# Performance work log

Measured on AMD Instinct MI355X. Metric: run time of the kernel, lower is better.

Reference implementation:

```python
import jax, jax.numpy as jnp
import numpy as np

B, S, D = 4, 2048, 1024
E, K, H = 8, 2, 2048  # experts, top_k, swiglu hidden (ff_multiplier=2.0)
EPS = 1e-8
RMS_EPS = 1e-6
ROPE_BASE = 10000.0


def setup_inputs() -> dict:
    key = jax.random.key(0)
    ks = jax.random.split(key, 6)
    scale_in = 1.0 / np.sqrt(D)
    scale_h = 1.0 / np.sqrt(H)
    return {
        "x": jax.random.normal(ks[0], (B, S, D), jnp.float32),
        "norm_w": jnp.ones((D,), jnp.float32),
        "router_W": jax.random.normal(ks[1], (E, D), jnp.float32) * scale_in,  # nn.Linear weight [E,D]
        "w1": jax.random.normal(ks[2], (E, H, D), jnp.float32) * scale_in,  # gate proj per expert
        "w3": jax.random.normal(ks[3], (E, H, D), jnp.float32) * scale_in,  # up proj per expert
        "w2": jax.random.normal(ks[4], (E, D, H), jnp.float32) * scale_h,   # down proj per expert
    }


def _rmsnorm(x, w):
    var = jnp.mean(jnp.square(x), axis=-1, keepdims=True)
    return x * jax.lax.rsqrt(var + RMS_EPS) * w


def _rope(x):
    # half-split rotary embedding over full embed dim; x: [B,S,D]
    d2 = D // 2
    inv_freq = 1.0 / (ROPE_BASE ** (jnp.arange(0, d2, dtype=jnp.float32) / d2))
    ang = jnp.arange(S, dtype=jnp.float32)[:, None] * inv_freq[None, :]  # [S,D/2]
    cos, sin = jnp.cos(ang), jnp.sin(ang)
    x1, x2 = x[..., :d2], x[..., d2:]
    return jnp.concatenate([x1 * cos - x2 * sin, x1 * sin + x2 * cos], axis=-1)


def reference(x, norm_w, router_W, w1, w3, w2):
    hidden = _rope(_rmsnorm(x, norm_w))  # [B,S,D]
    logits = jnp.einsum("bsd,ed->bse", hidden, router_W)
    probs = jax.nn.softmax(logits, axis=-1)
    # sparse top-k renormalized gates
    top_v, top_i = jax.lax.top_k(probs, K)  # [B,S,K]
    sparse = jnp.sum(jax.nn.one_hot(top_i, E, dtype=probs.dtype) * top_v[..., None], axis=-2)  # [B,S,E]
    gates = sparse / jnp.clip(jnp.sum(sparse, axis=-1, keepdims=True), EPS)
    # dense all-expert SwiGLU
    g = jnp.einsum("bsd,ehd->bseh", hidden, w1)
    u = jnp.einsum("bsd,ehd->bseh", hidden, w3)
    act = jax.nn.silu(g) * u
    expert_out = jnp.einsum("bseh,edh->bsed", act, w2)  # [B,S,E,D]
    mixed = jnp.sum(gates[..., None] * expert_out, axis=-2)
    return mixed + x
```

## Files before the change

kernel.cpp:

```cpp
#include <hip/hip_runtime.h>

#define TOKENS 8192
#define Dm 1024
#define Hm 2048
#define Sm 2048
#define D2 512
#define SLOTS 16384
#define PADU 256
#define SLOTPAD (SLOTS + 8*PADU)
#define NWE 16777216

#define OF_TAB 0ull
#define OF_HID (OF_TAB + (size_t)Sm*D2*8)
#define OF_ACT (OF_HID + (size_t)TOKENS*Dm*2)
#define OF_W1B (OF_ACT + (size_t)SLOTPAD*Hm*2)
#define OF_W3B (OF_W1B + (size_t)NWE*2)
#define OF_W2B (OF_W3B + (size_t)NWE*2)
#define OF_T2I (OF_W2B + (size_t)NWE*2)
#define OF_T2G (OF_T2I + (size_t)TOKENS*2*4)
#define OF_T2S (OF_T2G + (size_t)TOKENS*2*4)
#define OF_ST  (OF_T2S + (size_t)TOKENS*2*4)
#define OF_SG  (OF_ST + (size_t)SLOTPAD*4)
#define OF_MT  (OF_SG + (size_t)SLOTPAD*4)
#define OF_SO  (OF_MT + 1024)

typedef __bf16 bf16x8 __attribute__((ext_vector_type(8)));
typedef short  s16x8  __attribute__((ext_vector_type(8)));
typedef float  f32x4  __attribute__((ext_vector_type(4)));

__device__ __forceinline__ unsigned short f2bf(float f) {
    union { float f; unsigned u; } v; v.f = f;
    unsigned r = v.u + 0x7fffu + ((v.u >> 16) & 1u);
    return (unsigned short)(r >> 16);
}

__device__ __forceinline__ float bf2f(unsigned short u) {
    union { unsigned u; float f; } v; v.u = ((unsigned)u) << 16;
    return v.f;
}

__device__ __forceinline__ f32x4 mfma16(s16x8 a, s16x8 b, f32x4 c) {
    return __builtin_amdgcn_mfma_f32_16x16x32_bf16(
        __builtin_bit_cast(bf16x8, a), __builtin_bit_cast(bf16x8, b), c, 0, 0, 0);
}

__device__ __forceinline__ void gld16(const void* g, void* l) {
    __builtin_amdgcn_global_load_lds(
        (const __attribute__((address_space(1))) void*)g,
        (__attribute__((address_space(3))) void*)l, 16, 0, 0);
}

__device__ __forceinline__ int xcd_swz(int bid, int nwg) {
    int cpx = nwg >> 3;
    return (bid & 7) * cpx + (bid >> 3);
}

__global__ void k_init(int* slot_token, int* meta) {
    int i = blockIdx.x * 256 + threadIdx.x;
    if (i < SLOTPAD) slot_token[i] = -1;
    if (i < 8) meta[i] = 0;
}

__global__ __launch_bounds__(256) void k_convert3(
    const float* __restrict__ w1, const float* __restrict__ w3,
    const float* __restrict__ w2, unsigned short* __restrict__ d1,
    unsigned short* __restrict__ d3, unsigned short* __restrict__ d2)
{
    size_t i = ((size_t)blockIdx.x * 256 + threadIdx.x) * 8;
    const float* s; unsigned short* d;
    if (i < (size_t)NWE)            { s = w1; d = d1; }
    else if (i < 2ull * NWE)        { s = w3; d = d3; i -= (size_t)NWE; }
    else                            { s = w2; d = d2; i -= 2ull * NWE; }
    float4 a = *(const float4*)(s + i);
    float4 b = *(const float4*)(s + i + 4);
    s16x8 v;
    v[0]=(short)f2bf(a.x); v[1]=(short)f2bf(a.y); v[2]=(short)f2bf(a.z); v[3]=(short)f2bf(a.w);
    v[4]=(short)f2bf(b.x); v[5]=(short)f2bf(b.y); v[6]=(short)f2bf(b.z); v[7]=(short)f2bf(b.w);
    *(s16x8*)(d + i) = v;
}

__global__ void k_table(float2* tab) {
    int i = blockIdx.x * 256 + threadIdx.x;
    int s = i >> 9, j = i & 511;
    float inv = expf(-(float)j * (9.210340371976184f / 512.0f));
    float ang = (float)s * inv;
    tab[i] = make_float2(cosf(ang), sinf(ang));
}

__global__ __launch_bounds__(256) void k_token(
    const float* __restrict__ x, const float* __restrict__ nw,
    const float* __restrict__ rW, const float2* __restrict__ tab,
    unsigned short* __restrict__ hid,
    int* __restrict__ t2i, float* __restrict__ t2g)
{
    int t = blockIdx.x;
    int tid = threadIdx.x;
    int lane = tid & 63, wid = tid >> 6;
    int s = t & (Sm - 1);
    const float* xr = x + (size_t)t * Dm;

    float v0 = xr[tid], v1 = xr[tid + 256], v2 = xr[tid + 512], v3 = xr[tid + 768];
    float ss = v0*v0 + v1*v1 + v2*v2 + v3*v3;
    #pragma unroll
    for (int o = 32; o; o >>= 1) ss += __shfl_down(ss, o);
    __shared__ float red[4];
    if (lane == 0) red[wid] = ss;
    __syncthreads();
    float tot = red[0] + red[1] + red[2] + red[3];
    float rms = rsqrtf(tot * (1.0f / Dm) + 1e-6f);

    float n0 = v0 * rms * nw[tid];
    float n1 = v1 * rms * nw[tid + 256];
    float n2 = v2 * rms * nw[tid + 512];
    float n3 = v3 * rms * nw[tid + 768];

    float2 c0 = tab[s * D2 + tid];
    float2 c1 = tab[s * D2 + tid + 256];
    float h0 = n0 * c0.x - n2 * c0.y;
    float h2 = n0 * c0.y + n2 * c0.x;
    float h1 = n1 * c1.x - n3 * c1.y;
    float h3 = n1 * c1.y + n3 * c1.x;

    size_t base = (size_t)t * Dm;
    hid[base + tid]       = f2bf(h0);
    hid[base + tid + 256] = f2bf(h1);
    hid[base + tid + 512] = f2bf(h2);
    hid[base + tid + 768] = f2bf(h3);

    float p[8];
    #pragma unroll
    for (int e = 0; e < 8; e++) {
        const float* r = rW + (size_t)e * Dm;
        p[e] = h0 * r[tid] + h1 * r[tid + 256] + h2 * r[tid + 512] + h3 * r[tid + 768];
    }
    #pragma unroll
    for (int e = 0; e < 8; e++)
        #pragma unroll
        for (int o = 32; o; o >>= 1) p[e] += __shfl_down(p[e], o);
    __shared__ float rl[4][8];
    if (lane == 0) {
        #pragma unroll
        for (int e = 0; e < 8; e++) rl[wid][e] = p[e];
    }
    __syncthreads();
    if (tid == 0) {
        float lg[8];
        #pragma unroll
        for (int e = 0; e < 8; e++) lg[e] = rl[0][e] + rl[1][e] + rl[2][e] + rl[3][e];
        float m = lg[0];
        #pragma unroll
        for (int e = 1; e < 8; e++) m = fmaxf(m, lg[e]);
        int i0 = 0; float b0 = lg[0];
        #pragma unroll
        for (int e = 1; e < 8; e++) if (lg[e] > b0) { b0 = lg[e]; i0 = e; }
        int i1 = -1; float b1 = -3.0e38f;
        #pragma unroll
        for (int e = 0; e < 8; e++) if (e != i0 && lg[e] > b1) { b1 = lg[e]; i1 = e; }
        float p0 = expf(b0 - m), p1 = expf(b1 - m);
        float inv = 1.0f / (p0 + p1);
        t2i[2 * t] = i0; t2i[2 * t + 1] = i1;
        t2g[2 * t] = p0 * inv; t2g[2 * t + 1] = p1 * inv;
    }
}

__global__ __launch_bounds__(256) void k_hist(const int* __restrict__ t2i,
                                              int* __restrict__ meta) {
    __shared__ int h[8];
    int tid = threadIdx.x;
    if (tid < 8) h[tid] = 0;
    __syncthreads();
    int base = blockIdx.x * 512 + tid * 2;
    atomicAdd(&h[t2i[base]], 1);
    atomicAdd(&h[t2i[base + 1]], 1);
    __syncthreads();
    if (tid < 8) atomicAdd(&meta[tid], h[tid]);
}

__global__ void k_offsets(int* meta) {
    if (threadIdx.x == 0 && blockIdx.x == 0) {
        int acc = 0;
        for (int e = 0; e < 8; e++) {
            meta[8 + e] = acc;
            acc += ((meta[e] + PADU - 1) / PADU) * PADU;
        }
        meta[16] = acc;
        for (int e = 0; e < 8; e++) meta[17 + e] = meta[8 + e];
    }
}

__global__ __launch_bounds__(256) void k_place(
    const int* __restrict__ t2i, const float* __restrict__ t2g,
    int* __restrict__ slot_token, float* __restrict__ slot_gate,
    int* __restrict__ t2s, int* __restrict__ meta)
{
    __shared__ int lcnt[8];
    __shared__ int lbase[8];
    int tid = threadIdx.x;
    if (tid < 8) lcnt[tid] = 0;
    __syncthreads();
    int t = blockIdx.x * 256 + tid;
    int e0 = t2i[2 * t], e1 = t2i[2 * t + 1];
    int r0 = atomicAdd(&lcnt[e0], 1);
    int r1 = atomicAdd(&lcnt[e1], 1);
    __syncthreads();
    if (tid < 8) lbase[tid] = atomicAdd(&meta[17 + tid], lcnt[tid]);
    __syncthreads();
    int p0 = lbase[e0] + r0, p1 = lbase[e1] + r1;
    slot_token[p0] = t; slot_gate[p0] = t2g[2 * t];     t2s[2 * t]     = p0;
    slot_token[p1] = t; slot_gate[p1] = t2g[2 * t + 1]; t2s[2 * t + 1] = p1;
}

__global__ __launch_bounds__(512) void k_gemm1(
    const unsigned short* __restrict__ hid,
    const unsigned short* __restrict__ w1b, const unsigned short* __restrict__ w3b,
    const int* __restrict__ slot_token, unsigned short* __restrict__ act,
    const int* __restrict__ meta)
{
    int nwg = gridDim.x * gridDim.y;
    int bid = blockIdx.y * gridDim.x + blockIdx.x;
    int wg  = xcd_swz(bid, nwg);
    int bx  = wg % gridDim.x, by = wg / gridDim.x;

    int row0 = by * 256;
    if (row0 >= meta[16]) return;
    int e = 0;
    #pragma unroll
    for (int q = 1; q < 8; q++) if (row0 >= meta[8 + q]) e = q;
    int h0 = bx * 128;

    __shared__ unsigned short As[2][256 * 64];
    __shared__ unsigned short Bs[2][256 * 64];

    int tid = threadIdx.x, lane = tid & 63, w = tid >> 6;
    int wm = w >> 2, wn = w & 3;
    int wrow = wm * 128, wcol = wn * 32;
    int frow = lane & 15, q4 = lane >> 4;
    int rx = frow & 7;

    int grow = tid >> 3;
    int sslot = (tid & 7) ^ (grow & 7);

    const unsigned short* srcA[4];
    const unsigned short* srcB[4];
    #pragma unroll
    for (int g = 0; g < 4; g++) {
        int ra = g * 64 + grow;
        int tok = slot_token[row0 + ra];  if (tok < 0) tok = 0;
        srcA[g] = hid + (size_t)tok * Dm + sslot * 8;
        int rb = g * 64 + grow;
        srcB[g] = (rb < 128 ? w1b + ((size_t)e * Hm + h0 + rb) * Dm
                            : w3b + ((size_t)e * Hm + h0 + rb - 128) * Dm) + sslot * 8;
    }

    s16x8 a8[4][2], bG[2][2], bU[2][2];
    f32x4 accG[8][2] = {};
    f32x4 accU[8][2] = {};

#define SA(nb, g) gld16(srcA[g] + koff, (unsigned short*)&As[(nb)][(g) * 4096 + tid * 8])
#define SB(nb, g) gld16(srcB[g] + koff, (unsigned short*)&Bs[(nb)][(g) * 4096 + tid * 8])

#define RD_A(buf, half) do {                                                  \
    _Pragma("unroll") for (int i_ = 0; i_ < 4; i_++)                          \
    _Pragma("unroll") for (int kh_ = 0; kh_ < 2; kh_++) {                     \
        int sp_ = ((kh_ << 2) | q4) ^ rx;                                     \
        a8[i_][kh_] = *(const s16x8*)&As[(buf)][(wrow + (half) * 64 + i_ * 16 + frow) * 64 + sp_ * 8]; \
    } } while (0)

#define RD_B(buf, arr, base) do {                                             \
    _Pragma("unroll") for (int j_ = 0; j_ < 2; j_++)                          \
    _Pragma("unroll") for (int kh_ = 0; kh_ < 2; kh_++) {                     \
        int sp_ = ((kh_ << 2) | q4) ^ rx;                                     \
        arr[j_][kh_] = *(const s16x8*)&Bs[(buf)][((base) + wcol + j_ * 16 + frow) * 64 + sp_ * 8]; \
    } } while (0)

#define MFMA_Q(accX, bX, half) do {                                           \
    _Pragma("unroll") for (int i_ = 0; i_ < 4; i_++)                          \
    _Pragma("unroll") for (int j_ = 0; j_ < 2; j_++)                          \
    _Pragma("unroll") for (int kh_ = 0; kh_ < 2; kh_++)                       \
        accX[(half) * 4 + i_][j_] = mfma16(a8[i_][kh_], bX[j_][kh_], accX[(half) * 4 + i_][j_]); \
    } while (0)

#define PH_PRE  do { __builtin_amdgcn_s_barrier();                            \
    asm volatile("s_waitcnt lgkmcnt(0)" ::: "memory");                        \
    __builtin_amdgcn_sched_barrier(0);                                        \
    __builtin_amdgcn_s_setprio(1); } while (0)
#define PH_POST do { __builtin_amdgcn_s_setprio(0);                           \
    __builtin_amdgcn_s_barrier(); } while (0)

    {
        int koff = 0;
        #pragma unroll
        for (int g = 0; g < 4; g++) SA(0, g);
        #pragma unroll
        for (int g = 0; g < 4; g++) SB(0, g);
        asm volatile("s_waitcnt vmcnt(0)" ::: "memory");
        __builtin_amdgcn_s_barrier();
    }

    for (int kt = 0; kt < 16; ++kt) {
        int buf = kt & 1, nbuf = buf ^ 1;
        int koff = (kt + 1) * 64;
        bool st = kt < 15;
        RD_A(buf, 0); RD_B(buf, bG, 0);
        if (st) { SA(nbuf, 0); SA(nbuf, 1); SA(nbuf, 2); }
        PH_PRE; MFMA_Q(accG, bG, 0); PH_POST;
        RD_B(buf, bU, 128);
        if (st) { SA(nbuf, 3); SB(nbuf, 0); SB(nbuf, 1); }
        PH_PRE; MFMA_Q(accU, bU, 0); PH_POST;
        RD_A(buf, 1);
        if (st) { SB(nbuf, 2); SB(nbuf, 3); }
        PH_PRE; MFMA_Q(accG, bG, 1); PH_POST;
        __builtin_amdgcn_s_setprio(1);
        MFMA_Q(accU, bU, 1);
        __builtin_amdgcn_s_setprio(0);
        asm volatile("s_waitcnt vmcnt(0)" ::: "memory");
        __builtin_amdgcn_s_barrier();
        __builtin_amdgcn_sched_barrier(0);
    }

#undef SA
#undef SB
#undef RD_A
#undef RD_B
#undef MFMA_Q
#undef PH_PRE
#undef PH_POST

    #pragma unroll
    for (int m = 0; m < 8; m++)
        #pragma unroll
        for (int j = 0; j < 2; j++)
            #pragma unroll
            for (int r = 0; r < 4; r++) {
                int sr = row0 + wrow + m * 16 + q4 * 4 + r;
                int hc = h0 + wcol + j * 16 + frow;
                float g = accG[m][j][r], u = accU[m][j][r];
                float a = g / (1.0f + expf(-g)) * u;
                act[(size_t)sr * Hm + hc] = f2bf(a);
            }
}

__global__ __launch_bounds__(256) void k_gemm2(
    const unsigned short* __restrict__ act, const unsigned short* __restrict__ w2b,
    const float* __restrict__ slot_gate,
    unsigned short* __restrict__ sout, const int* __restrict__ meta)
{
    int nwg = gridDim.x * gridDim.y;
    int bid = blockIdx.y * gridDim.x + blockIdx.x;
    int wg  = xcd_swz(bid, nwg);
    int bx  = wg % gridDim.x, by = wg / gridDim.x;

    int row0 = by * 128;
    if (row0 >= meta[16]) return;
    int e = 0;
    #pragma unroll
    for (int q = 1; q < 8; q++) if (row0 >= meta[8 + q]) e = q;
    int d0 = bx * 128;

    __shared__ unsigned short As[2][128 * 64];
    __shared__ unsigned short Bs[2][128 * 64];
    __shared__ float sgat[128];

    int tid = threadIdx.x, lane = tid & 63, w = tid >> 6;
    int wm = w >> 1, wn = w & 1;
    int frow = lane & 15, q4 = lane >> 4;
    int rx = frow & 7;

    if (tid < 128) sgat[tid] = slot_gate[row0 + tid];

    int r7 = (tid >> 3) & 7;
    int sslot = (tid & 7) ^ r7;

    const unsigned short* srcA[4];
    const unsigned short* srcB[4];
    #pragma unroll
    for (int i = 0; i < 4; i++) {
        int rr = i * 32 + (tid >> 3);
        srcA[i] = act + (size_t)(row0 + rr) * Hm + sslot * 8;
        srcB[i] = w2b + ((size_t)e * Dm + d0 + rr) * Hm + sslot * 8;
    }

    f32x4 acc[4][4] = {};

#define STAGE2(buf, k0) do {                                                  \
    unsigned short* la_ = &As[(buf)][tid * 8];                                \
    unsigned short* lb_ = &Bs[(buf)][tid * 8];                                \
    _Pragma("unroll")                                                         \
    for (int i_ = 0; i_ < 4; i_++) {                                          \
        gld16(srcA[i_] + (k0), la_ + i_ * 2048);                              \
        gld16(srcB[i_] + (k0), lb_ + i_ * 2048);                              \
    } } while (0)

#define COMP2(buf) do {                                                       \
    _Pragma("unroll")                                                         \
    for (int h_ = 0; h_ < 2; h_++) {                                          \
        int sp_ = ((h_ << 2) | q4) ^ rx;                                      \
        s16x8 am_[4], bn_[4];                                                 \
        _Pragma("unroll")                                                     \
        for (int i_ = 0; i_ < 4; i_++)                                        \
            am_[i_] = *(const s16x8*)&As[(buf)][(wm * 64 + i_ * 16 + frow) * 64 + sp_ * 8]; \
        _Pragma("unroll")                                                     \
        for (int j_ = 0; j_ < 4; j_++)                                        \
            bn_[j_] = *(const s16x8*)&Bs[(buf)][(wn * 64 + j_ * 16 + frow) * 64 + sp_ * 8]; \
        _Pragma("unroll")                                                     \
        for (int i_ = 0; i_ < 4; i_++)                                        \
            _Pragma("unroll")                                                 \
            for (int j_ = 0; j_ < 4; j_++)                                    \
                acc[i_][j_] = mfma16(am_[i_], bn_[j_], acc[i_][j_]);          \
    } } while (0)

    STAGE2(0, 0);
    #pragma unroll 2
    for (int kt = 0; kt < 31; ++kt) {
        STAGE2((kt + 1) & 1, (kt + 1) * 64);
        asm volatile("s_waitcnt vmcnt(8)" ::: "memory");
        __builtin_amdgcn_s_barrier();
        __builtin_amdgcn_sched_barrier(0);
        COMP2(kt & 1);
        __builtin_amdgcn_sched_barrier(0);
        __builtin_amdgcn_s_barrier();
    }
    asm volatile("s_waitcnt vmcnt(0)" ::: "memory");
    __builtin_amdgcn_s_barrier();
    __builtin_amdgcn_sched_barrier(0);
    COMP2(1);

#undef STAGE2
#undef COMP2

    #pragma unroll
    for (int i = 0; i < 4; i++) {
        #pragma unroll
        for (int r = 0; r < 4; r++) {
            int srl = wm * 64 + i * 16 + q4 * 4 + r;
            float gate = sgat[srl];
            size_t rb = (size_t)(row0 + srl) * Dm;
            #pragma unroll
            for (int j = 0; j < 4; j++) {
                int dc = d0 + wn * 64 + j * 16 + frow;
                sout[rb + dc] = f2bf(gate * acc[i][j][r]);
            }
        }
    }
}

__global__ __launch_bounds__(256) void k_final(
    const float* __restrict__ x, const unsigned short* __restrict__ sout,
    const int* __restrict__ t2s, float* __restrict__ out)
{
    int t = blockIdx.x;
    int tid = threadIdx.x;
    int s0 = t2s[2 * t], s1 = t2s[2 * t + 1];
    const float4*  xr = (const float4*)(x + (size_t)t * Dm);
    const ushort4* a  = (const ushort4*)(sout + (size_t)s0 * Dm);
    const ushort4* b  = (const ushort4*)(sout + (size_t)s1 * Dm);
    float4* o = (float4*)(out + (size_t)t * Dm);
    float4 xv = xr[tid];
    ushort4 av = a[tid], bv = b[tid];
    float4 r;
    r.x = xv.x + bf2f(av.x) + bf2f(bv.x);
    r.y = xv.y + bf2f(av.y) + bf2f(bv.y);
    r.z = xv.z + bf2f(av.z) + bf2f(bv.z);
    r.w = xv.w + bf2f(av.w) + bf2f(bv.w);
    o[tid] = r;
}

extern "C" void kernel_launch(void* const* d_in, const int* in_sizes, int n_in,
                              void* d_out, int out_size, void* d_ws, size_t ws_size,
                              hipStream_t stream) {
    const float* x  = (const float*)d_in[0];
    const float* nw = (const float*)d_in[1];
    const float* rW = (const float*)d_in[2];
    const float* w1 = (const float*)d_in[3];
    const float* w3 = (const float*)d_in[4];
    const float* w2 = (const float*)d_in[5];
    float* out = (float*)d_out;
    char* ws = (char*)d_ws;

    float2* tab = (float2*)(ws + OF_TAB);
    unsigned short* hid = (unsigned short*)(ws + OF_HID);
    unsigned short* act = (unsigned short*)(ws + OF_ACT);
    unsigned short* w1b = (unsigned short*)(ws + OF_W1B);
    unsigned short* w3b = (unsigned short*)(ws + OF_W3B);
    unsigned short* w2b = (unsigned short*)(ws + OF_W2B);
    int*   t2i  = (int*)(ws + OF_T2I);
    float* t2g  = (float*)(ws + OF_T2G);
    int*   t2s  = (int*)(ws + OF_T2S);
    int*   stok = (int*)(ws + OF_ST);
    float* sgat = (float*)(ws + OF_SG);
    int*   meta = (int*)(ws + OF_MT);
    unsigned short* sout = (unsigned short*)(ws + OF_SO);

    k_init<<<(SLOTPAD + 255) / 256, 256, 0, stream>>>(stok, meta);
    k_table<<<(Sm * D2) / 256, 256, 0, stream>>>(tab);
    k_convert3<<<3 * (NWE / (256 * 8)), 256, 0, stream>>>(w1, w3, w2, w1b, w3b, w2b);
    k_token<<<TOKENS, 256, 0, stream>>>(x, nw, rW, tab, hid, t2i, t2g);
    k_hist<<<32, 256, 0, stream>>>(t2i, meta);
    k_offsets<<<1, 64, 0, stream>>>(meta);
    k_place<<<TOKENS / 256, 256, 0, stream>>>(t2i, t2g, stok, sgat, t2s, meta);

    dim3 g1(Hm / 128, SLOTPAD / 256);
    k_gemm1<<<g1, 512, 0, stream>>>(hid, w1b, w3b, stok, act, meta);
    dim3 g2(Dm / 128, SLOTPAD / 128);
    k_gemm2<<<g2, 256, 0, stream>>>(act, w2b, sgat, sout, meta);
    k_final<<<TOKENS, 256, 0, stream>>>(x, sout, t2s, out);
}
```

Measured before the change: 383.0 us.

## Fuse prep kernels into one launch and restructure gemm1 prefetch pipeline

Merges the init, weight conversion and per-token norm/rope/router kernels into a single block-partitioned launch, cutting launch count and letting the token and conversion work run concurrently. Rewrites the gemm1 main loop so all next-tile global-to-LDS loads are issued up front, followed by a partial vmcnt wait and one barrier pair per iteration. This replaces the interleaved phase barriers and priority toggling, with the last tile peeled out of the loop. gemm1 also gets a launch_bounds occupancy hint of 2 blocks, which may constrain registers and risk spills.

```diff
diff --git a/kernel.cpp b/kernel.cpp
--- a/kernel.cpp
+++ b/kernel.cpp
@@ -24,6 +24,10 @@
 #define OF_MT  (OF_SG + (size_t)SLOTPAD*4)
 #define OF_SO  (OF_MT + 1024)
 
+#define PREP_TOKEN 8192
+#define PREP_CONV  (PREP_TOKEN + 3 * (NWE / (256 * 8)))
+#define PREP_INIT  (PREP_CONV + (SLOTPAD + 255) / 256)
+
 typedef __bf16 bf16x8 __attribute__((ext_vector_type(8)));
 typedef short  s16x8  __attribute__((ext_vector_type(8)));
 typedef float  f32x4  __attribute__((ext_vector_type(4)));
@@ -53,30 +57,6 @@
 __device__ __forceinline__ int xcd_swz(int bid, int nwg) {
     int cpx = nwg >> 3;
     return (bid & 7) * cpx + (bid >> 3);
-}
-
-__global__ void k_init(int* slot_token, int* meta) {
-    int i = blockIdx.x * 256 + threadIdx.x;
-    if (i < SLOTPAD) slot_token[i] = -1;
-    if (i < 8) meta[i] = 0;
-}
-
-__global__ __launch_bounds__(256) void k_convert3(
-    const float* __restrict__ w1, const float* __restrict__ w3,
-    const float* __restrict__ w2, unsigned short* __restrict__ d1,
-    unsigned short* __restrict__ d3, unsigned short* __restrict__ d2)
-{
-    size_t i = ((size_t)blockIdx.x * 256 + threadIdx.x) * 8;
-    const float* s; unsigned short* d;
-    if (i < (size_t)NWE)            { s = w1; d = d1; }
-    else if (i < 2ull * NWE)        { s = w3; d = d3; i -= (size_t)NWE; }
-    else                            { s = w2; d = d2; i -= 2ull * NWE; }
-    float4 a = *(const float4*)(s + i);
-    float4 b = *(const float4*)(s + i + 4);
-    s16x8 v;
-    v[0]=(short)f2bf(a.x); v[1]=(short)f2bf(a.y); v[2]=(short)f2bf(a.z); v[3]=(short)f2bf(a.w);
-    v[4]=(short)f2bf(b.x); v[5]=(short)f2bf(b.y); v[6]=(short)f2bf(b.z); v[7]=(short)f2bf(b.w);
-    *(s16x8*)(d + i) = v;
 }
 
 __global__ void k_table(float2* tab) {
@@ -87,14 +67,44 @@
     tab[i] = make_float2(cosf(ang), sinf(ang));
 }
 
-__global__ __launch_bounds__(256) void k_token(
+__global__ __launch_bounds__(256) void k_prep(
     const float* __restrict__ x, const float* __restrict__ nw,
     const float* __restrict__ rW, const float2* __restrict__ tab,
-    unsigned short* __restrict__ hid,
-    int* __restrict__ t2i, float* __restrict__ t2g)
+    const float* __restrict__ w1, const float* __restrict__ w3,
+    const float* __restrict__ w2,
+    unsigned short* __restrict__ hid, int* __restrict__ t2i,
+    float* __restrict__ t2g,
+    unsigned short* __restrict__ d1, unsigned short* __restrict__ d3,
+    unsigned short* __restrict__ d2,
+    int* __restrict__ slot_token, int* __restrict__ meta)
 {
-    int t = blockIdx.x;
+    __shared__ float red[4];
+    __shared__ float rl[4][8];
+    int bid = blockIdx.x;
     int tid = threadIdx.x;
+
+    if (bid >= PREP_CONV) {
+        int i = (bid - PREP_CONV) * 256 + tid;
+        if (i < SLOTPAD) slot_token[i] = -1;
+        if (i < 8) meta[i] = 0;
+        return;
+    }
+    if (bid >= PREP_TOKEN) {
+        size_t i = ((size_t)(bid - PREP_TOKEN) * 256 + tid) * 8;
+        const float* s; unsigned short* d;
+        if (i < (size_t)NWE)            { s = w1; d = d1; }
+        else if (i < 2ull * NWE)        { s = w3; d = d3; i -= (size_t)NWE; }
+        else                            { s = w2; d = d2; i -= 2ull * NWE; }
+        float4 a = *(const float4*)(s + i);
+        float4 b = *(const float4*)(s + i + 4);
+        s16x8 v;
+        v[0]=(short)f2bf(a.x); v[1]=(short)f2bf(a.y); v[2]=(short)f2bf(a.z); v[3]=(short)f2bf(a.w);
+        v[4]=(short)f2bf(b.x); v[5]=(short)f2bf(b.y); v[6]=(short)f2bf(b.z); v[7]=(short)f2bf(b.w);
+        *(s16x8*)(d + i) = v;
+        return;
+    }
+
+    int t = bid;
     int lane = tid & 63, wid = tid >> 6;
     int s = t & (Sm - 1);
     const float* xr = x + (size_t)t * Dm;
@@ -103,7 +113,6 @@
     float ss = v0*v0 + v1*v1 + v2*v2 + v3*v3;
     #pragma unroll
     for (int o = 32; o; o >>= 1) ss += __shfl_down(ss, o);
-    __shared__ float red[4];
     if (lane == 0) red[wid] = ss;
     __syncthreads();
     float tot = red[0] + red[1] + red[2] + red[3];
@@ -137,7 +146,6 @@
     for (int e = 0; e < 8; e++)
         #pragma unroll
         for (int o = 32; o; o >>= 1) p[e] += __shfl_down(p[e], o);
-    __shared__ float rl[4][8];
     if (lane == 0) {
         #pragma unroll
         for (int e = 0; e < 8; e++) rl[wid][e] = p[e];
@@ -210,7 +218,7 @@
     slot_token[p1] = t; slot_gate[p1] = t2g[2 * t + 1]; t2s[2 * t + 1] = p1;
 }
 
-__global__ __launch_bounds__(512) void k_gemm1(
+__global__ __launch_bounds__(512, 2) void k_gemm1(
     const unsigned short* __restrict__ hid,
     const unsigned short* __restrict__ w1b, const unsigned short* __restrict__ w3b,
     const int* __restrict__ slot_token, unsigned short* __restrict__ act,
@@ -280,12 +288,16 @@
         accX[(half) * 4 + i_][j_] = mfma16(a8[i_][kh_], bX[j_][kh_], accX[(half) * 4 + i_][j_]); \
     } while (0)
 
-#define PH_PRE  do { __builtin_amdgcn_s_barrier();                            \
-    asm volatile("s_waitcnt lgkmcnt(0)" ::: "memory");                        \
-    __builtin_amdgcn_sched_barrier(0);                                        \
-    __builtin_amdgcn_s_setprio(1); } while (0)
-#define PH_POST do { __builtin_amdgcn_s_setprio(0);                           \
-    __builtin_amdgcn_s_barrier(); } while (0)
+#define COMP1(buf) do {                                                       \
+    RD_A(buf, 0);                                                             \
+    RD_B(buf, bG, 0);                                                         \
+    MFMA_Q(accG, bG, 0);                                                      \
+    RD_B(buf, bU, 128);                                                       \
+    MFMA_Q(accU, bU, 0);                                                      \
+    RD_A(buf, 1);                                                             \
+    MFMA_Q(accG, bG, 1);                                                      \
+    MFMA_Q(accU, bU, 1);                                                      \
+    } while (0)
 
     {
         int koff = 0;
@@ -293,38 +305,35 @@
         for (int g = 0; g < 4; g++) SA(0, g);
         #pragma unroll
         for (int g = 0; g < 4; g++) SB(0, g);
-        asm volatile("s_waitcnt vmcnt(0)" ::: "memory");
-        __builtin_amdgcn_s_barrier();
-    }
-
-    for (int kt = 0; kt < 16; ++kt) {
+    }
+
+    for (int kt = 0; kt < 15; ++kt) {
         int buf = kt & 1, nbuf = buf ^ 1;
-        int koff = (kt + 1) * 64;
-        bool st = kt < 15;
-        RD_A(buf, 0); RD_B(buf, bG, 0);
-        if (st) { SA(nbuf, 0); SA(nbuf, 1); SA(nbuf, 2); }
-        PH_PRE; MFMA_Q(accG, bG, 0); PH_POST;
-        RD_B(buf, bU, 128);
-        if (st) { SA(nbuf, 3); SB(nbuf, 0); SB(nbuf, 1); }
-        PH_PRE; MFMA_Q(accU, bU, 0); PH_POST;
-        RD_A(buf, 1);
-        if (st) { SB(nbuf, 2); SB(nbuf, 3); }
-        PH_PRE; MFMA_Q(accG, bG, 1); PH_POST;
-        __builtin_amdgcn_s_setprio(1);
-        MFMA_Q(accU, bU, 1);
-        __builtin_amdgcn_s_setprio(0);
-        asm volatile("s_waitcnt vmcnt(0)" ::: "memory");
+        {
+            int koff = (kt + 1) * 64;
+            #pragma unroll
+            for (int g = 0; g < 4; g++) SA(nbuf, g);
+            #pragma unroll
+            for (int g = 0; g < 4; g++) SB(nbuf, g);
+        }
+        asm volatile("s_waitcnt vmcnt(8)" ::: "memory");
         __builtin_amdgcn_s_barrier();
         __builtin_amdgcn_sched_barrier(0);
-    }
+        COMP1(buf);
+        __builtin_amdgcn_sched_barrier(0);
+        __builtin_amdgcn_s_barrier();
+    }
+    asm volatile("s_waitcnt vmcnt(0)" ::: "memory");
+    __builtin_amdgcn_s_barrier();
+    __builtin_amdgcn_sched_barrier(0);
+    COMP1(1);
 
 #undef SA
 #undef SB
 #undef RD_A
 #undef RD_B
 #undef MFMA_Q
-#undef PH_PRE
-#undef PH_POST
+#undef COMP1
 
     #pragma unroll
     for (int m = 0; m < 8; m++)
@@ -491,10 +500,10 @@
     int*   meta = (int*)(ws + OF_MT);
     unsigned short* sout = (unsigned short*)(ws + OF_SO);
 
-    k_init<<<(SLOTPAD + 255) / 256, 256, 0, stream>>>(stok, meta);
     k_table<<<(Sm * D2) / 256, 256, 0, stream>>>(tab);
-    k_convert3<<<3 * (NWE / (256 * 8)), 256, 0, stream>>>(w1, w3, w2, w1b, w3b, w2b);
-    k_token<<<TOKENS, 256, 0, stream>>>(x, nw, rW, tab, hid, t2i, t2g);
+    k_prep<<<PREP_INIT, 256, 0, stream>>>(x, nw, rW, tab, w1, w3, w2,
+                                          hid, t2i, t2g, w1b, w3b, w2b,
+                                          stok, meta);
     k_hist<<<32, 256, 0, stream>>>(t2i, meta);
     k_offsets<<<1, 64, 0, stream>>>(meta);
     k_place<<<TOKENS / 256, 256, 0, stream>>>(t2i, t2g, stok, sgat, t2s, meta);
```

Result: no change. 388.1 us (+1.3%).
